# Performance work log

Hardware: AMD Instinct MI355X
Metric: run time of the kernel (lower is better)

Reference implementation:

```python
import jax, jax.numpy as jnp
import numpy as np

B, N, L, D = 128, 1024, 512, 64


def setup_inputs() -> dict:
    key = jax.random.key(0)
    k1, k2 = jax.random.split(key)
    text_outputs = jax.random.normal(k1, (B, N, D), dtype=jnp.float32)
    image_outputs = jax.random.normal(k2, (B, L, D), dtype=jnp.float32)
    rng = np.random.RandomState(0)
    ntok = rng.randint(N // 4, N + 1, size=B)
    nreg = rng.randint(L // 4, L + 1, size=B)
    text_mask = (np.arange(N)[None, :] < ntok[:, None]).astype(np.float32)
    image_mask = (np.arange(L)[None, :] < nreg[:, None]).astype(np.float32)
    # impostor indices (torch code samples these with np.random inside forward;
    # here they are fixed constants for determinism), guaranteed != own index
    I_imp = rng.randint(0, B, size=B)
    S_imp = rng.randint(0, B, size=B)
    ar = np.arange(B)
    I_imp = np.where(I_imp == ar, (I_imp + 1) % B, I_imp).astype(np.int32)
    S_imp = np.where(S_imp == ar, (S_imp + 1) % B, S_imp).astype(np.int32)
    return {
        "text_outputs": text_outputs,
        "image_outputs": image_outputs,
        "text_mask": jnp.asarray(text_mask),
        "image_mask": jnp.asarray(image_mask),
        "I_imp_idx": jnp.asarray(I_imp),
        "S_imp_idx": jnp.asarray(S_imp),
    }


def _mean_max_sim(T, I, tmask, imask):
    # T: (N, D) tokens, I: (L, D) regions; masks select the ragged valid prefix.
    M = jnp.einsum('nd,ld->nl', T, I)                       # matchmap (N, L)
    neg = jnp.finfo(M.dtype).min
    mx = jnp.max(jnp.where(imask[None, :] > 0, M, neg), axis=1)  # max over regions
    return jnp.sum(mx * tmask) / jnp.sum(tmask)             # mean over valid tokens


def reference(text_outputs, image_outputs, text_mask, image_mask, I_imp_idx, S_imp_idx, margin=1.0):
    sim = jax.vmap(_mean_max_sim)
    anchor = sim(text_outputs, image_outputs, text_mask, image_mask)            # (B,)
    Simpsim = sim(text_outputs[S_imp_idx], image_outputs, text_mask[S_imp_idx], image_mask)
    Iimpsim = sim(text_outputs, image_outputs[I_imp_idx], text_mask, image_mask[I_imp_idx])
    # scalar per-sample hinge: term added only when margin+imp-anchor > 0 == relu
    per_sample = jax.nn.relu(margin + Iimpsim - anchor) + jax.nn.relu(margin + Simpsim - anchor)
    loss = jnp.sum(per_sample) / text_outputs.shape[0]
    return loss[None]  # torch returns shape (1,)
```

## Files before the change

### kernel.cpp

```cpp
#include <hip/hip_runtime.h>

#define B 128
#define N 1024
#define L 512
#define D 64

typedef float f32x4 __attribute__((ext_vector_type(4)));
typedef short bf16x8 __attribute__((ext_vector_type(8)));


__global__ void init_kernel(const float* __restrict__ tmask,
                            const float* __restrict__ imask,
                            float* __restrict__ sims,
                            int* __restrict__ cnts) {
    int blk = blockIdx.x;
    int tid = threadIdx.x;
    __shared__ float red[256];
    float s = 0.f;
    if (blk < B) {
        for (int i = tid; i < N; i += 256) s += tmask[blk * N + i];
    } else {
        int r = blk - B;
        for (int i = tid; i < L; i += 256) s += imask[r * L + i];
    }
    red[tid] = s;
    __syncthreads();
    for (int off = 128; off > 0; off >>= 1) {
        if (tid < off) red[tid] += red[tid + off];
        __syncthreads();
    }
    if (tid == 0) cnts[blk] = (int)(red[0] + 0.5f);
    if (blk < B && tid < 3) sims[tid * B + blk] = 0.f;
}

__device__ inline unsigned int pack_bf16(float lo, float hi) {
    unsigned int a = __float_as_uint(lo), b = __float_as_uint(hi);
    a = (a + 0x7fffu + ((a >> 16) & 1u)) >> 16;
    b = (b + 0x7fffu + ((b >> 16) & 1u)) & 0xffff0000u;
    return a | b;
}

#define RSTRIDE 72

__global__ __launch_bounds__(256) void sim_kernel(
        const float* __restrict__ T, const float* __restrict__ I,
        const int* __restrict__ Iimp, const int* __restrict__ Simp,
        const int* __restrict__ cnts, float* __restrict__ sims) {
    int blk = blockIdx.x;
    int chunk = blk & 3;
    int bs = blk >> 2;
    int b = bs & (B - 1);
    int s = bs >> 7;
    int Tb = b, Ib = b;
    if (s == 1) Tb = Simp[b];
    else if (s == 2) Ib = Iimp[b];
    int ntok = cnts[Tb];
    int nreg = cnts[B + Ib];
    int tok0 = chunk * 256;
    if (tok0 >= ntok) return;

    int tid = threadIdx.x;
    int w = tid >> 6;
    int lane = tid & 63;
    int q = lane >> 4;
    int c = lane & 15;

    __shared__ unsigned short ldsI[64 * RSTRIDE];
    __shared__ float wsum[4];

    int wt0 = tok0 + w * 64;
    bf16x8 afrag[4][2];
#pragma unroll
    for (int tt = 0; tt < 4; ++tt) {
        const float* trow = T + ((size_t)Tb * N + wt0 + tt * 16 + c) * D;
#pragma unroll
        for (int h = 0; h < 2; ++h) {
            const float4* p = (const float4*)(trow + h * 32 + q * 8);
            float4 f0 = p[0], f1 = p[1];
            unsigned int u[4];
            u[0] = pack_bf16(f0.x, f0.y);
            u[1] = pack_bf16(f0.z, f0.w);
            u[2] = pack_bf16(f1.x, f1.y);
            u[3] = pack_bf16(f1.z, f1.w);
            afrag[tt][h] = *(bf16x8*)u;
        }
    }

    float mx[4][4];
#pragma unroll
    for (int tt = 0; tt < 4; ++tt)
#pragma unroll
        for (int i = 0; i < 4; ++i) mx[tt][i] = -3.4e38f;

    const float* Ibase = I + (size_t)Ib * L * D;

    for (int r0 = 0; r0 < nreg; r0 += 64) {
        {
            int r = tid >> 2;
            int dseg = (tid & 3) * 16;
            int gr = r0 + r;
            float4 f[4];
            if (gr < nreg) {
                const float4* p = (const float4*)(Ibase + (size_t)gr * D + dseg);
#pragma unroll
                for (int i = 0; i < 4; ++i) f[i] = p[i];
            } else {
#pragma unroll
                for (int i = 0; i < 4; ++i) f[i] = make_float4(0.f, 0.f, 0.f, 0.f);
            }
            unsigned int u[8];
#pragma unroll
            for (int i = 0; i < 4; ++i) {
                u[2 * i]     = pack_bf16(f[i].x, f[i].y);
                u[2 * i + 1] = pack_bf16(f[i].z, f[i].w);
            }
            uint4* dst = (uint4*)&ldsI[r * RSTRIDE + dseg];
            dst[0] = *(uint4*)&u[0];
            dst[1] = *(uint4*)&u[4];
        }
        __syncthreads();

        int nrt = nreg - r0;
        nrt = nrt > 64 ? 4 : ((nrt + 15) >> 4);
#pragma unroll 1
        for (int rt = 0; rt < nrt; ++rt) {
            int rr = rt * 16 + c;
            bf16x8 bf0 = *(bf16x8*)&ldsI[rr * RSTRIDE + q * 8];
            bf16x8 bf1 = *(bf16x8*)&ldsI[rr * RSTRIDE + 32 + q * 8];
            bool valid = (r0 + rt * 16 + c) < nreg;
#pragma unroll
            for (int tt = 0; tt < 4; ++tt) {
                f32x4 acc = {0.f, 0.f, 0.f, 0.f};
                acc = __builtin_amdgcn_mfma_f32_16x16x32_bf16(afrag[tt][0], bf0, acc, 0, 0, 0);
                acc = __builtin_amdgcn_mfma_f32_16x16x32_bf16(afrag[tt][1], bf1, acc, 0, 0, 0);
                if (valid) {
#pragma unroll
                    for (int i = 0; i < 4; ++i) mx[tt][i] = fmaxf(mx[tt][i], acc[i]);
                }
            }
        }
        __syncthreads();
    }

#pragma unroll
    for (int m = 1; m < 16; m <<= 1) {
#pragma unroll
        for (int tt = 0; tt < 4; ++tt)
#pragma unroll
            for (int i = 0; i < 4; ++i)
                mx[tt][i] = fmaxf(mx[tt][i], __shfl_xor(mx[tt][i], m));
    }

    float lsum = 0.f;
    if (c == 0) {
#pragma unroll
        for (int tt = 0; tt < 4; ++tt)
#pragma unroll
            for (int i = 0; i < 4; ++i) {
                int row = wt0 + tt * 16 + q * 4 + i;
                if (row < ntok) lsum += mx[tt][i];
            }
    }
    for (int off = 32; off > 0; off >>= 1) lsum += __shfl_down(lsum, off);
    if (lane == 0) wsum[w] = lsum;
    __syncthreads();
    if (tid == 0) {
        float tot = wsum[0] + wsum[1] + wsum[2] + wsum[3];
        atomicAdd(&sims[s * B + b], tot / (float)ntok);
    }
}

__global__ void loss_kernel(const float* __restrict__ sims,
                            float* __restrict__ out) {
    int tid = threadIdx.x;
    float anc = sims[tid];
    float simp = sims[B + tid];
    float iimp = sims[2 * B + tid];
    float per = fmaxf(1.f + iimp - anc, 0.f) + fmaxf(1.f + simp - anc, 0.f);
    for (int off = 32; off > 0; off >>= 1) per += __shfl_down(per, off);
    __shared__ float w2[2];
    if ((tid & 63) == 0) w2[tid >> 6] = per;
    __syncthreads();
    if (tid == 0) out[0] = (w2[0] + w2[1]) / (float)B;
}

extern "C" void kernel_launch(void* const* d_in, const int* in_sizes, int n_in,
                              void* d_out, int out_size, void* d_ws, size_t ws_size,
                              hipStream_t stream) {
    const float* T     = (const float*)d_in[0];
    const float* I     = (const float*)d_in[1];
    const float* tmask = (const float*)d_in[2];
    const float* imask = (const float*)d_in[3];
    const int*   Iimp  = (const int*)d_in[4];
    const int*   Simp  = (const int*)d_in[5];
    float* sims = (float*)d_ws;
    int*   cnts = (int*)((char*)d_ws + 3 * B * sizeof(float));

    init_kernel<<<2 * B, 256, 0, stream>>>(tmask, imask, sims, cnts);
    sim_kernel<<<3 * B * (N / 256), 256, 0, stream>>>(T, I, Iimp, Simp, cnts, sims);
    loss_kernel<<<1, 128, 0, stream>>>(sims, (float*)d_out);
}
```

Baseline: 132.5 us.

## Stage whole image in LDS once per pair and fuse mask counting

Each block now handles one (sample, pair) with all token chunks, loading the full valid image (bf16, MFMA-fragment order) into 64KB LDS once instead of reconverting it per 256-token chunk. The init kernel is removed: mask counts are computed inside the sim kernel, and atomics are replaced with direct stores. The grid drops from 1536 to 384 blocks, so per-block work is serialized over token chunks and GPU occupancy and load balance may suffer, especially with 64KB LDS per block.

```diff
diff --git a/kernel.cpp b/kernel.cpp
--- a/kernel.cpp
+++ b/kernel.cpp
@@ -8,31 +8,6 @@
 typedef float f32x4 __attribute__((ext_vector_type(4)));
 typedef short bf16x8 __attribute__((ext_vector_type(8)));
 
-
-__global__ void init_kernel(const float* __restrict__ tmask,
-                            const float* __restrict__ imask,
-                            float* __restrict__ sims,
-                            int* __restrict__ cnts) {
-    int blk = blockIdx.x;
-    int tid = threadIdx.x;
-    __shared__ float red[256];
-    float s = 0.f;
-    if (blk < B) {
-        for (int i = tid; i < N; i += 256) s += tmask[blk * N + i];
-    } else {
-        int r = blk - B;
-        for (int i = tid; i < L; i += 256) s += imask[r * L + i];
-    }
-    red[tid] = s;
-    __syncthreads();
-    for (int off = 128; off > 0; off >>= 1) {
-        if (tid < off) red[tid] += red[tid + off];
-        __syncthreads();
-    }
-    if (tid == 0) cnts[blk] = (int)(red[0] + 0.5f);
-    if (blk < B && tid < 3) sims[tid * B + blk] = 0.f;
-}
-
 __device__ inline unsigned int pack_bf16(float lo, float hi) {
     unsigned int a = __float_as_uint(lo), b = __float_as_uint(hi);
     a = (a + 0x7fffu + ((a >> 16) & 1u)) >> 16;
@@ -40,24 +15,17 @@
     return a | b;
 }
 
-#define RSTRIDE 72
-
-__global__ __launch_bounds__(256) void sim_kernel(
+__global__ __launch_bounds__(256, 2) void sim_kernel(
         const float* __restrict__ T, const float* __restrict__ I,
+        const float* __restrict__ tmask, const float* __restrict__ imask,
         const int* __restrict__ Iimp, const int* __restrict__ Simp,
-        const int* __restrict__ cnts, float* __restrict__ sims) {
+        float* __restrict__ sims) {
     int blk = blockIdx.x;
-    int chunk = blk & 3;
-    int bs = blk >> 2;
-    int b = bs & (B - 1);
-    int s = bs >> 7;
+    int s = blk >> 7;
+    int b = blk & (B - 1);
     int Tb = b, Ib = b;
     if (s == 1) Tb = Simp[b];
     else if (s == 2) Ib = Iimp[b];
-    int ntok = cnts[Tb];
-    int nreg = cnts[B + Ib];
-    int tok0 = chunk * 256;
-    if (tok0 >= ntok) return;
 
     int tid = threadIdx.x;
     int w = tid >> 6;
@@ -65,109 +33,131 @@
     int q = lane >> 4;
     int c = lane & 15;
 
-    __shared__ unsigned short ldsI[64 * RSTRIDE];
-    __shared__ float wsum[4];
+    __shared__ unsigned short ldsI[L * D];
+    float* redf = (float*)ldsI;
 
-    int wt0 = tok0 + w * 64;
-    bf16x8 afrag[4][2];
+    float ts = 0.f, is = 0.f;
+    {
+        const float* tm = tmask + (size_t)Tb * N;
+        for (int i = tid; i < N; i += 256) ts += tm[i];
+        const float* im = imask + (size_t)Ib * L;
+        for (int i = tid; i < L; i += 256) is += im[i];
+    }
+    for (int off = 32; off > 0; off >>= 1) {
+        ts += __shfl_down(ts, off);
+        is += __shfl_down(is, off);
+    }
+    if (lane == 0) { redf[w] = ts; redf[4 + w] = is; }
+    __syncthreads();
+    int ntok = (int)(redf[0] + redf[1] + redf[2] + redf[3] + 0.5f);
+    int nreg = (int)(redf[4] + redf[5] + redf[6] + redf[7] + 0.5f);
+    __syncthreads();
+
+    int full_rt = nreg >> 4;
+    int rem = nreg & 15;
+    int nrt = full_rt + (rem ? 1 : 0);
+    int nchunk = nrt * 128;
+    const float* Ibase = I + (size_t)Ib * L * D;
+    for (int ci = tid; ci < nchunk; ci += 256) {
+        int rt = ci >> 7;
+        int h = (ci >> 6) & 1;
+        int ln = ci & 63;
+        int r = rt * 16 + (ln & 15);
+        int dbase = h * 32 + (ln >> 4) * 8;
+        uint4 outv = make_uint4(0u, 0u, 0u, 0u);
+        if (r < nreg) {
+            const float4* p = (const float4*)(Ibase + (size_t)r * D + dbase);
+            float4 f0 = p[0], f1 = p[1];
+            outv.x = pack_bf16(f0.x, f0.y);
+            outv.y = pack_bf16(f0.z, f0.w);
+            outv.z = pack_bf16(f1.x, f1.y);
+            outv.w = pack_bf16(f1.z, f1.w);
+        }
+        *(uint4*)((char*)ldsI + (size_t)ci * 16) = outv;
+    }
+    __syncthreads();
+
+    const char* ldsB = (const char*)ldsI + (size_t)lane * 16;
+    float bsum = 0.f;
+    for (int tok0 = 0; tok0 < ntok; tok0 += 256) {
+        int wt0 = tok0 + w * 64;
+        bf16x8 afrag[4][2];
 #pragma unroll
-    for (int tt = 0; tt < 4; ++tt) {
-        const float* trow = T + ((size_t)Tb * N + wt0 + tt * 16 + c) * D;
+        for (int tt = 0; tt < 4; ++tt) {
+            const float* trow = T + ((size_t)Tb * N + wt0 + tt * 16 + c) * D;
 #pragma unroll
-        for (int h = 0; h < 2; ++h) {
-            const float4* p = (const float4*)(trow + h * 32 + q * 8);
-            float4 f0 = p[0], f1 = p[1];
-            unsigned int u[4];
-            u[0] = pack_bf16(f0.x, f0.y);
-            u[1] = pack_bf16(f0.z, f0.w);
-            u[2] = pack_bf16(f1.x, f1.y);
-            u[3] = pack_bf16(f1.z, f1.w);
-            afrag[tt][h] = *(bf16x8*)u;
+            for (int h = 0; h < 2; ++h) {
+                const float4* p = (const float4*)(trow + h * 32 + q * 8);
+                float4 f0 = p[0], f1 = p[1];
+                unsigned int u[4];
+                u[0] = pack_bf16(f0.x, f0.y);
+                u[1] = pack_bf16(f0.z, f0.w);
+                u[2] = pack_bf16(f1.x, f1.y);
+                u[3] = pack_bf16(f1.z, f1.w);
+                afrag[tt][h] = *(bf16x8*)u;
+            }
         }
-    }
 
-    float mx[4][4];
+        float mx[4][4];
 #pragma unroll
-    for (int tt = 0; tt < 4; ++tt)
+        for (int tt = 0; tt < 4; ++tt)
 #pragma unroll
-        for (int i = 0; i < 4; ++i) mx[tt][i] = -3.4e38f;
+            for (int i = 0; i < 4; ++i) mx[tt][i] = -3.0e38f;
 
-    const float* Ibase = I + (size_t)Ib * L * D;
-
-    for (int r0 = 0; r0 < nreg; r0 += 64) {
-        {
-            int r = tid >> 2;
-            int dseg = (tid & 3) * 16;
-            int gr = r0 + r;
-            float4 f[4];
-            if (gr < nreg) {
-                const float4* p = (const float4*)(Ibase + (size_t)gr * D + dseg);
-#pragma unroll
-                for (int i = 0; i < 4; ++i) f[i] = p[i];
-            } else {
-#pragma unroll
-                for (int i = 0; i < 4; ++i) f[i] = make_float4(0.f, 0.f, 0.f, 0.f);
-            }
-            unsigned int u[8];
-#pragma unroll
-            for (int i = 0; i < 4; ++i) {
-                u[2 * i]     = pack_bf16(f[i].x, f[i].y);
-                u[2 * i + 1] = pack_bf16(f[i].z, f[i].w);
-            }
-            uint4* dst = (uint4*)&ldsI[r * RSTRIDE + dseg];
-            dst[0] = *(uint4*)&u[0];
-            dst[1] = *(uint4*)&u[4];
-        }
-        __syncthreads();
-
-        int nrt = nreg - r0;
-        nrt = nrt > 64 ? 4 : ((nrt + 15) >> 4);
 #pragma unroll 1
-        for (int rt = 0; rt < nrt; ++rt) {
-            int rr = rt * 16 + c;
-            bf16x8 bf0 = *(bf16x8*)&ldsI[rr * RSTRIDE + q * 8];
-            bf16x8 bf1 = *(bf16x8*)&ldsI[rr * RSTRIDE + 32 + q * 8];
-            bool valid = (r0 + rt * 16 + c) < nreg;
+        for (int rt = 0; rt < full_rt; ++rt) {
+            bf16x8 b0 = *(const bf16x8*)(ldsB + (size_t)(rt * 2 + 0) * 1024);
+            bf16x8 b1 = *(const bf16x8*)(ldsB + (size_t)(rt * 2 + 1) * 1024);
 #pragma unroll
             for (int tt = 0; tt < 4; ++tt) {
                 f32x4 acc = {0.f, 0.f, 0.f, 0.f};
-                acc = __builtin_amdgcn_mfma_f32_16x16x32_bf16(afrag[tt][0], bf0, acc, 0, 0, 0);
-                acc = __builtin_amdgcn_mfma_f32_16x16x32_bf16(afrag[tt][1], bf1, acc, 0, 0, 0);
+                acc = __builtin_amdgcn_mfma_f32_16x16x32_bf16(afrag[tt][0], b0, acc, 0, 0, 0);
+                acc = __builtin_amdgcn_mfma_f32_16x16x32_bf16(afrag[tt][1], b1, acc, 0, 0, 0);
+#pragma unroll
+                for (int i = 0; i < 4; ++i) mx[tt][i] = fmaxf(mx[tt][i], acc[i]);
+            }
+        }
+        if (rem) {
+            bf16x8 b0 = *(const bf16x8*)(ldsB + (size_t)(full_rt * 2 + 0) * 1024);
+            bf16x8 b1 = *(const bf16x8*)(ldsB + (size_t)(full_rt * 2 + 1) * 1024);
+            bool valid = c < rem;
+#pragma unroll
+            for (int tt = 0; tt < 4; ++tt) {
+                f32x4 acc = {0.f, 0.f, 0.f, 0.f};
+                acc = __builtin_amdgcn_mfma_f32_16x16x32_bf16(afrag[tt][0], b0, acc, 0, 0, 0);
+                acc = __builtin_amdgcn_mfma_f32_16x16x32_bf16(afrag[tt][1], b1, acc, 0, 0, 0);
                 if (valid) {
 #pragma unroll
                     for (int i = 0; i < 4; ++i) mx[tt][i] = fmaxf(mx[tt][i], acc[i]);
                 }
             }
         }
-        __syncthreads();
+
+#pragma unroll
+        for (int m = 1; m < 16; m <<= 1) {
+#pragma unroll
+            for (int tt = 0; tt < 4; ++tt)
+#pragma unroll
+                for (int i = 0; i < 4; ++i)
+                    mx[tt][i] = fmaxf(mx[tt][i], __shfl_xor(mx[tt][i], m));
+        }
+        if (c == 0) {
+#pragma unroll
+            for (int tt = 0; tt < 4; ++tt)
+#pragma unroll
+                for (int i = 0; i < 4; ++i) {
+                    int row = wt0 + tt * 16 + q * 4 + i;
+                    if (row < ntok) bsum += mx[tt][i];
+                }
+        }
     }
 
-#pragma unroll
-    for (int m = 1; m < 16; m <<= 1) {
-#pragma unroll
-        for (int tt = 0; tt < 4; ++tt)
-#pragma unroll
-            for (int i = 0; i < 4; ++i)
-                mx[tt][i] = fmaxf(mx[tt][i], __shfl_xor(mx[tt][i], m));
-    }
-
-    float lsum = 0.f;
-    if (c == 0) {
-#pragma unroll
-        for (int tt = 0; tt < 4; ++tt)
-#pragma unroll
-            for (int i = 0; i < 4; ++i) {
-                int row = wt0 + tt * 16 + q * 4 + i;
-                if (row < ntok) lsum += mx[tt][i];
-            }
-    }
-    for (int off = 32; off > 0; off >>= 1) lsum += __shfl_down(lsum, off);
-    if (lane == 0) wsum[w] = lsum;
+    for (int off = 32; off > 0; off >>= 1) bsum += __shfl_down(bsum, off);
     __syncthreads();
-    if (tid == 0) {
-        float tot = wsum[0] + wsum[1] + wsum[2] + wsum[3];
-        atomicAdd(&sims[s * B + b], tot / (float)ntok);
-    }
+    if (lane == 0) redf[8 + w] = bsum;
+    __syncthreads();
+    if (tid == 0)
+        sims[s * B + b] = (redf[8] + redf[9] + redf[10] + redf[11]) / (float)ntok;
 }
 
 __global__ void loss_kernel(const float* __restrict__ sims,
@@ -194,9 +184,7 @@
     const int*   Iimp  = (const int*)d_in[4];
     const int*   Simp  = (const int*)d_in[5];
     float* sims = (float*)d_ws;
-    int*   cnts = (int*)((char*)d_ws + 3 * B * sizeof(float));
 
-    init_kernel<<<2 * B, 256, 0, stream>>>(tmask, imask, sims, cnts);
-    sim_kernel<<<3 * B * (N / 256), 256, 0, stream>>>(T, I, Iimp, Simp, cnts, sims);
+    sim_kernel<<<3 * B, 256, 0, stream>>>(T, I, tmask, imask, Iimp, Simp, sims);
     loss_kernel<<<1, 128, 0, stream>>>(sims, (float*)d_out);
 }
```

Result: slower. 138.4 us (+4.4%).
